# Kernel tuning notes

Measured on AMD Instinct MI355X. Metric: run time of the kernel, lower is better.

## Reference

```python
import jax, jax.numpy as jnp
import numpy as np

IN_CH, HID, OUT_CH = 1, 16, 1

def _conv(x, w, b, pad):
    # x: [B,C,H,W], w: [O,I,kh,kw], b: [O]
    y = jax.lax.conv_general_dilated(
        x, w, window_strides=(1, 1), padding=[(pad, pad), (pad, pad)],
        dimension_numbers=('NCHW', 'OIHW', 'NCHW'))
    return y + b[None, :, None, None]

def setup_inputs() -> dict:
    key = jax.random.key(0)
    ks = jax.random.split(key, 8)
    def w_init(k, shape):
        fan_in = shape[1] * shape[2] * shape[3]
        return jax.random.normal(k, shape, dtype=jnp.float32) * (1.0 / np.sqrt(fan_in))
    B, H, W = 32, 256, 256
    return {
        'x': jax.random.normal(ks[0], (B, IN_CH, H, W), dtype=jnp.float32),
        'w_perceive': w_init(ks[1], (HID * 2, IN_CH + HID, 3, 3)),
        'b_perceive': jnp.zeros((HID * 2,), jnp.float32),
        'w_up1': w_init(ks[2], (HID, HID * 2, 1, 1)),
        'b_up1': jnp.zeros((HID,), jnp.float32),
        'w_up2': w_init(ks[3], (HID, HID, 1, 1)),
        'b_up2': jnp.zeros((HID,), jnp.float32),
        'w_tau': w_init(ks[4], (HID, IN_CH + HID * 2, 3, 3)),
        'b_tau_conv': jnp.zeros((HID,), jnp.float32),
        'b_tau': jnp.ones((1, HID, 1, 1), jnp.float32) * 1.5,
        'w_read': w_init(ks[5], (OUT_CH, HID, 1, 1)),
        'b_read': jnp.zeros((OUT_CH,), jnp.float32),
        'n_steps': 10,
    }

def reference(x, w_perceive, b_perceive, w_up1, b_up1, w_up2, b_up2,
              w_tau, b_tau_conv, b_tau, w_read, b_read, n_steps):
    B, _, H, W = x.shape
    state = jnp.zeros((B, HID, H, W), dtype=x.dtype)

    def step(state, _):
        combined = jnp.concatenate([x, state], axis=1)          # [B, in+hid, H, W]
        perception = _conv(combined, w_perceive, b_perceive, 1)  # [B, 2*hid, H, W]
        h1 = jax.nn.relu(_conv(perception, w_up1, b_up1, 0))
        delta = _conv(h1, w_up2, b_up2, 0)                       # [B, hid, H, W]
        tau_input = jnp.concatenate([x, state, delta], axis=1)  # [B, in+2*hid, H, W]
        tau_logit = _conv(tau_input, w_tau, b_tau_conv, 1) + b_tau
        beta = jnp.clip(jax.nn.sigmoid(tau_logit), 0.01, 0.99)
        return beta * state + (1.0 - beta) * delta, None

    state, _ = jax.lax.scan(step, state, None, length=n_steps)
    return jax.nn.sigmoid(_conv(state, w_read, b_read, 0))
```

## Files before the change

kernel.cpp:

```cpp
#include <hip/hip_runtime.h>
#include <hip/hip_bf16.h>
#include <math.h>


#define B_   32
#define H_   256
#define W_   256
#define PIT  40
#define XPP  260

typedef unsigned short ushort_t;
typedef __attribute__((ext_vector_type(8))) short short8;
typedef __attribute__((ext_vector_type(4))) float float4v;

__device__ __forceinline__ unsigned fbits(float f) {
    union { float f; unsigned u; } v; v.f = f; return v.u;
}
__device__ __forceinline__ ushort_t f2bu(float f) {
    return (ushort_t)((fbits(f) + 0x8000u) >> 16);
}
__device__ __forceinline__ unsigned pack2(float lo, float hi) {
    union { __hip_bfloat162 h; unsigned u; } v;
    v.h = __float22bfloat162_rn(make_float2(lo, hi));
    return v.u;
}
__device__ __forceinline__ float bu2f(ushort_t u) {
    union { unsigned i; float f; } v; v.i = ((unsigned)u) << 16; return v.f;
}
__device__ __forceinline__ float lo2f(unsigned u) {
    union { unsigned i; float f; } v; v.i = u << 16; return v.f;
}
__device__ __forceinline__ float hi2f(unsigned u) {
    union { unsigned i; float f; } v; v.i = u & 0xFFFF0000u; return v.f;
}

__global__ void prep(
    const float* __restrict__ wp,
    const float* __restrict__ wu1,
    const float* __restrict__ bu1,
    const float* __restrict__ bp,
    const float* __restrict__ wu2,
    const float* __restrict__ wt,
    const float* __restrict__ btc,
    const float* __restrict__ bt,
    ushort_t* __restrict__ wh1p,
    ushort_t* __restrict__ wu2f,
    ushort_t* __restrict__ wtxf,
    ushort_t* __restrict__ wtn,
    float* __restrict__ scal)
{
    __shared__ float Weff[16 * 153];
    const int tid = threadIdx.x;

    for (int i = tid; i < 16 * 153; i += 256) {
        int j = i / 153, rem = i % 153, c = rem / 9, t = rem % 9;
        float s = 0.f;
        for (int o = 0; o < 32; ++o)
            s += wu1[j * 32 + o] * wp[o * 153 + c * 9 + t];
        Weff[i] = s;
    }
    if (tid < 16) {
        float s = bu1[tid];
        for (int o = 0; o < 32; ++o) s += wu1[tid * 32 + o] * bp[o];
        scal[tid] = s;
    }
    if (tid < 16) scal[32 + tid] = btc[tid] + bt[tid];
    if (tid < 16) scal[48 + tid] = wt[tid * 297 + 8];
    __syncthreads();

    if (tid < 16) scal[16 + tid] = Weff[tid * 153 + 8];

    for (int i = tid; i < 4 * 64 * 8; i += 256) {
        int ii = i >> 9, lane = (i >> 3) & 63, j = i & 7;
        int n = lane & 15, kk = ((lane >> 4) << 3) + j;
        int tap = 2 * ii + (kk >> 4), ch = kk & 15;
        wh1p[i] = f2bu(Weff[n * 153 + (ch + 1) * 9 + tap]);
    }
    for (int i = tid; i < 512; i += 256) {
        int lane = i >> 3, j = i & 7;
        int n = lane & 15, k = ((lane >> 4) << 3) + j;
        float v = 0.f;
        if (k < 16)       v = Weff[n * 153 + (k + 1) * 9 + 8];
        else if (k < 24)  v = Weff[n * 153 + (k - 16)];
        else if (k == 24) v = Weff[n * 153 + 8];
        wh1p[2048 + i] = f2bu(v);
    }
    for (int i = tid; i < 512; i += 256) {
        int lane = i >> 3, j = i & 7;
        int n = lane & 15, k = ((lane >> 4) << 3) + j;
        wu2f[i] = (k < 16) ? f2bu(wu2[n * 16 + k]) : (ushort_t)0;
    }
    for (int i = tid; i < 512; i += 256) {
        int lane = i >> 3, j = i & 7;
        int n = lane & 15, k = ((lane >> 4) << 3) + j;
        wtxf[i] = (k < 8) ? f2bu(wt[n * 297 + k]) : (ushort_t)0;
    }
    for (int i = tid; i < 9 * 64 * 8; i += 256) {
        int t = i / 512, lane = (i / 8) % 64, j = i % 8;
        int n = lane & 15, k = ((lane >> 4) << 3) + j;
        int c = (k < 16) ? (17 + k) : (k - 15);
        wtn[i] = f2bu(wt[n * 297 + c * 9 + t]);
    }
}

__global__ __launch_bounds__(256) void precompute_xp8(
    const float* __restrict__ x,
    ushort_t* __restrict__ xp8)
{
    int idx = blockIdx.x * 256 + threadIdx.x;
    if (idx >= B_ * XPP * XPP) return;
    int b  = idx / (XPP * XPP), rem = idx - b * (XPP * XPP);
    int by = rem / XPP, bx = rem - by * XPP;
    int gy = by - 2, gx = bx - 2;
    const float* xb = x + (size_t)b * 65536;
    short8 v;
#pragma unroll
    for (int t = 0; t < 8; ++t) {
        int yy = gy + t / 3, xx = gx + t % 3;
        bool in = ((unsigned)yy < 256u) & ((unsigned)xx < 256u);
        v[t] = in ? (short)f2bu(xb[yy * 256 + xx]) : (short)0;
    }
    *(short8*)(xp8 + (size_t)idx * 8) = v;
}

__global__ __launch_bounds__(256) void nca_step(
    const ushort_t* __restrict__ stIn,
    ushort_t* __restrict__ stOut,
    const ushort_t* __restrict__ xp8g,
    const ushort_t* __restrict__ wh1p,
    const ushort_t* __restrict__ wu2f,
    const ushort_t* __restrict__ wtxf,
    const ushort_t* __restrict__ wtn,
    const float* __restrict__ scal,
    const float* __restrict__ bu2G,
    const float* __restrict__ wrd,
    const float* __restrict__ brd,
    float* __restrict__ outg,
    int first, int last)
{
    __shared__ ushort_t comb[400 * PIT];

    const int tid  = threadIdx.x;
    const int w    = tid >> 6, lane = tid & 63;
    const int m    = lane & 15, q = lane >> 4;
    const int och  = q * 4;
    const int flat = ((int)blockIdx.z << 8) | ((int)blockIdx.y << 4) | (int)blockIdx.x;
    const int nf   = ((flat & 7) << 10) | (flat >> 3);
    const int bxi  = nf & 15, byi = (nf >> 4) & 15, bzi = nf >> 8;
    const int gx0  = bxi * 16, gy0 = byi * 16;
    const size_t pb = (size_t)bzi * 65536;
    const size_t xpb = (size_t)bzi * (XPP * XPP);
    const short8 z8 = {0, 0, 0, 0, 0, 0, 0, 0};
    const float4v z4 = {0.f, 0.f, 0.f, 0.f};

    const bool interior = (bxi >= 1) & (bxi <= 14) & (byi >= 1) & (byi <= 14);

    short8 wh1r[5], wtnr[9];
#pragma unroll
    for (int i = 0; i < 5; ++i) wh1r[i] = *(const short8*)(wh1p + (i * 64 + lane) * 8);
#pragma unroll
    for (int t = 0; t < 9; ++t) wtnr[t] = *(const short8*)(wtn + (t * 64 + lane) * 8);
    const short8 wu2r = *(const short8*)(wu2f + lane * 8);
    const short8 wtxr = *(const short8*)(wtxf + lane * 8);

    float4v beff4, bu24, wr4, tb4, wtx84;
#pragma unroll
    for (int r = 0; r < 4; ++r) {
        beff4[r] = scal[och + r];
        tb4[r]   = scal[32 + och + r];
        wtx84[r] = scal[48 + och + r];
        bu24[r]  = bu2G[och + r];
        wr4[r]   = wrd[och + r];
    }
    const float br = brd[0];

    const int sel = q >> 1;
    int offp[4];
#pragma unroll
    for (int ii = 0; ii < 4; ++ii) {
        int tA = 2 * ii, tB = 2 * ii + 1;
        int oA = ((tA / 3) * 20 + (tA % 3)) * PIT;
        int oB = ((tB / 3) * 20 + (tB % 3)) * PIT;
        offp[ii] = sel ? oB : oA;
    }
    const int chOff = 16 + (q & 1) * 8;
    const int t8off = (2 * 20 + 2) * PIT;
    const int off5  = (q == 0) ? (t8off + 16) : (q == 1) ? (t8off + 24)
                    : (q == 2) ? 32 : (t8off + 32);

    const int bpA = ((m + (q << 5)) & 63) << 2;

    if (interior & (first == 0)) {
        for (int p = tid; p < 400; p += 256) {
            int ry = p / 20, rx = p - ry * 20;
            ushort_t* row = comb + p * PIT;
            const ushort_t* sp = stIn
                + (pb + (size_t)(gy0 + ry - 2) * 256 + (gx0 + rx - 2)) * 16;
            *(short8*)(row + 16) = *(const short8*)(sp);
            *(short8*)(row + 24) = *(const short8*)(sp + 8);
            *(short8*)(row + 32) = *(const short8*)(
                xp8g + (xpb + (size_t)(gy0 + ry) * XPP + (gx0 + rx)) * 8);
        }
    } else {
        for (int p = tid; p < 400; p += 256) {
            int ry = p / 20, rx = p - ry * 20;
            int gy = gy0 + ry - 2, gx = gx0 + rx - 2;
            ushort_t* row = comb + p * PIT;
            bool in = ((unsigned)gy < 256u) & ((unsigned)gx < 256u);
            if (in && !first) {
                const ushort_t* sp = stIn + (pb + gy * 256 + gx) * 16;
                *(short8*)(row + 16) = *(const short8*)(sp);
                *(short8*)(row + 24) = *(const short8*)(sp + 8);
            } else {
                *(short8*)(row + 16) = z8; *(short8*)(row + 24) = z8;
            }
            *(short8*)(row + 32) = *(const short8*)(
                xp8g + (xpb + (size_t)(gy0 + ry) * XPP + (gx0 + rx)) * 8);
        }
    }
    __syncthreads();

    {
        int raw = w * 16 + m;
        int py = raw / 18, px = raw - (raw / 18) * 18;
        for (int i = 0; i < 6; ++i) {
            int g = w + 4 * i; if (g >= 21) break;
            bool vld = raw < 324;
            int pyc = vld ? py : 17, pxc = vld ? px : 17;
            const ushort_t* abase = comb + (pyc * 20 + pxc) * PIT;
            float4v acc = z4;
            __builtin_amdgcn_s_setprio(1);
#pragma unroll
            for (int ii = 0; ii < 4; ++ii) {
                short8 b = *(const short8*)(abase + offp[ii] + chOff);
                acc = __builtin_amdgcn_mfma_f32_16x16x32_bf16(wh1r[ii], b, acc, 0, 0, 0);
            }
            {
                short8 b = *(const short8*)(abase + off5);
                acc = __builtin_amdgcn_mfma_f32_16x16x32_bf16(wh1r[4], b, acc, 0, 0, 0);
            }
            __builtin_amdgcn_s_setprio(0);
            uint2 hv;
            hv.x = pack2(fmaxf(acc[0] + beff4[0], 0.f),
                         fmaxf(acc[1] + beff4[1], 0.f));
            hv.y = pack2(fmaxf(acc[2] + beff4[2], 0.f),
                         fmaxf(acc[3] + beff4[3], 0.f));
            union { int i4[4]; short8 s8; } bb;
            bb.i4[0] = __builtin_amdgcn_ds_bpermute(bpA,      (int)hv.x);
            bb.i4[1] = __builtin_amdgcn_ds_bpermute(bpA,      (int)hv.y);
            bb.i4[2] = __builtin_amdgcn_ds_bpermute(bpA + 64, (int)hv.x);
            bb.i4[3] = __builtin_amdgcn_ds_bpermute(bpA + 64, (int)hv.y);
            float4v d = __builtin_amdgcn_mfma_f32_16x16x32_bf16(wu2r, bb.s8, z4, 0, 0, 0);
            uint2 dv;
            dv.x = pack2(d[0] + bu24[0], d[1] + bu24[1]);
            dv.y = pack2(d[2] + bu24[2], d[3] + bu24[3]);
            if (!interior) {
                int gy = gy0 - 1 + pyc, gx = gx0 - 1 + pxc;
                bool im = ((unsigned)gy < 256u) & ((unsigned)gx < 256u);
                if (!im) { dv.x = 0u; dv.y = 0u; }
            }
            if (vld)
                *(uint2*)(comb + ((pyc + 1) * 20 + (pxc + 1)) * PIT + och) = dv;
            raw += 64; px += 10; py += 3;
            if (px >= 18) { px -= 18; py += 1; }
        }
    }
    __syncthreads();

    {
        const int w4 = w * 4;
#define LDROW(r, dx) (*(const short8*)(comb + (((r) * 20) + (m + 1 + (dx))) * PIT + q * 8))
        short8 Ta0 = LDROW(w4 + 1, 0), Ta1 = LDROW(w4 + 1, 1), Ta2 = LDROW(w4 + 1, 2);
        short8 Tb0 = LDROW(w4 + 2, 0), Tb1 = LDROW(w4 + 2, 1), Tb2 = LDROW(w4 + 2, 2);
#pragma unroll
        for (int i = 0; i < 4; ++i) {
            int g = w4 + i;
            short8 Tc0 = LDROW(g + 3, 0), Tc1 = LDROW(g + 3, 1), Tc2 = LDROW(g + 3, 2);
            short8 bx = *(const short8*)(comb + ((g + 1) * 20 + (m + 1)) * PIT + 32);
            const ushort_t* cpx = comb + ((g + 2) * 20 + (m + 2)) * PIT;
            float x8c = bu2f(comb[((g + 3) * 20 + (m + 3)) * PIT + 32]);
            uint2 su = *(const uint2*)(cpx + 16 + och);
            uint2 du = *(const uint2*)(cpx + och);
            float4v acc = z4;
            __builtin_amdgcn_s_setprio(1);
            acc = __builtin_amdgcn_mfma_f32_16x16x32_bf16(wtnr[0], Ta0, acc, 0, 0, 0);
            acc = __builtin_amdgcn_mfma_f32_16x16x32_bf16(wtnr[1], Ta1, acc, 0, 0, 0);
            acc = __builtin_amdgcn_mfma_f32_16x16x32_bf16(wtnr[2], Ta2, acc, 0, 0, 0);
            acc = __builtin_amdgcn_mfma_f32_16x16x32_bf16(wtnr[3], Tb0, acc, 0, 0, 0);
            acc = __builtin_amdgcn_mfma_f32_16x16x32_bf16(wtnr[4], Tb1, acc, 0, 0, 0);
            acc = __builtin_amdgcn_mfma_f32_16x16x32_bf16(wtnr[5], Tb2, acc, 0, 0, 0);
            acc = __builtin_amdgcn_mfma_f32_16x16x32_bf16(wtnr[6], Tc0, acc, 0, 0, 0);
            acc = __builtin_amdgcn_mfma_f32_16x16x32_bf16(wtnr[7], Tc1, acc, 0, 0, 0);
            acc = __builtin_amdgcn_mfma_f32_16x16x32_bf16(wtnr[8], Tc2, acc, 0, 0, 0);
            acc = __builtin_amdgcn_mfma_f32_16x16x32_bf16(wtxr,   bx,  acc, 0, 0, 0);
            __builtin_amdgcn_s_setprio(0);
            int gy = gy0 + g;
            const size_t pix = pb + gy * 256 + gx0 + m;
            float sold[4] = { lo2f(su.x), hi2f(su.x), lo2f(su.y), hi2f(su.y) };
            float dvv[4]  = { lo2f(du.x), hi2f(du.x), lo2f(du.y), hi2f(du.y) };
            float sn[4];
#pragma unroll
            for (int r = 0; r < 4; ++r) {
                float tl  = acc[r] + tb4[r] + x8c * wtx84[r];
                float e   = __expf(-tl);
                float bta = __builtin_amdgcn_rcpf(1.f + e);
                bta = fminf(fmaxf(bta, 0.01f), 0.99f);
                sn[r] = dvv[r] + bta * (sold[r] - dvv[r]);
            }
            if (!last) {
                uint2 o;
                o.x = pack2(sn[0], sn[1]); o.y = pack2(sn[2], sn[3]);
                *(uint2*)(stOut + pix * 16 + och) = o;
            } else {
                float v = sn[0] * wr4[0] + sn[1] * wr4[1]
                        + sn[2] * wr4[2] + sn[3] * wr4[3];
                v += __shfl_xor(v, 16);
                v += __shfl_xor(v, 32);
                if (q == 0) {
                    float eo = __expf(-(v + br));
                    outg[pix] = __builtin_amdgcn_rcpf(1.f + eo);
                }
            }
            Ta0 = Tb0; Ta1 = Tb1; Ta2 = Tb2;
            Tb0 = Tc0; Tb1 = Tc1; Tb2 = Tc2;
        }
#undef LDROW
    }
}

extern "C" void kernel_launch(void* const* d_in, const int* in_sizes, int n_in,
                              void* d_out, int out_size, void* d_ws, size_t ws_size,
                              hipStream_t stream)
{
    const float* x          = (const float*)d_in[0];
    const float* w_perceive = (const float*)d_in[1];
    const float* b_perceive = (const float*)d_in[2];
    const float* w_up1      = (const float*)d_in[3];
    const float* b_up1      = (const float*)d_in[4];
    const float* w_up2      = (const float*)d_in[5];
    const float* b_up2      = (const float*)d_in[6];
    const float* w_tau      = (const float*)d_in[7];
    const float* b_tau_conv = (const float*)d_in[8];
    const float* b_tau      = (const float*)d_in[9];
    const float* w_read     = (const float*)d_in[10];
    const float* b_read     = (const float*)d_in[11];
    float* out = (float*)d_out;

    const size_t stateElems = (size_t)B_ * H_ * W_ * 16;
    const size_t xp8Elems   = (size_t)B_ * XPP * XPP * 8;

    ushort_t* stA  = (ushort_t*)d_ws;
    ushort_t* stB  = stA + stateElems;
    ushort_t* xp8g = stB + stateElems;
    ushort_t* wh1p = xp8g + xp8Elems;
    ushort_t* wu2f = wh1p + 2560;
    ushort_t* wtxf = wu2f + 512;
    ushort_t* wtn  = wtxf + 512;
    float*    scal = (float*)(wtn + 4608);

    const size_t needBytes = (2 * stateElems + xp8Elems
                              + 2560 + 512 + 512 + 4608) * sizeof(ushort_t)
                           + 64 * sizeof(float);
    if (ws_size < needBytes) return;

    prep<<<dim3(1), dim3(256), 0, stream>>>(
        w_perceive, w_up1, b_up1, b_perceive, w_up2, w_tau,
        b_tau_conv, b_tau, wh1p, wu2f, wtxf, wtn, scal);
    precompute_xp8<<<dim3((B_ * XPP * XPP + 255) / 256), dim3(256), 0, stream>>>(
        x, xp8g);

    ushort_t* cur = stA;
    ushort_t* nxt = stB;
    for (int s = 0; s < 10; ++s) {
        nca_step<<<dim3(16, 16, 32), dim3(256), 0, stream>>>(
            cur, nxt, xp8g, wh1p, wu2f, wtxf, wtn, scal, b_up2,
            w_read, b_read, out, (s == 0) ? 1 : 0, (s == 9) ? 1 : 0);
        ushort_t* t = cur; cur = nxt; nxt = t;
    }
}
```

Before: 731.0 us.

## Fuse two NCA steps per launch using wider halo tile in shared memory

Each launch now computes two update steps: the shared tile grows from 20x20 to 24x24 with a 4-pixel halo, the first step's state is recomputed over a 20x20 region and written back to shared memory, then the second step runs as before. This halves the number of launches and the global state reads and writes between steps. In exchange it adds redundant halo computation, more shared memory per block, and a launch_bounds occupancy hint of 3.

```diff
diff --git a/kernel.cpp b/kernel.cpp
--- a/kernel.cpp
+++ b/kernel.cpp
@@ -7,7 +7,7 @@
 #define H_   256
 #define W_   256
 #define PIT  40
-#define XPP  260
+#define XPP  264
 
 typedef unsigned short ushort_t;
 typedef __attribute__((ext_vector_type(8))) short short8;
@@ -111,7 +111,7 @@
     if (idx >= B_ * XPP * XPP) return;
     int b  = idx / (XPP * XPP), rem = idx - b * (XPP * XPP);
     int by = rem / XPP, bx = rem - by * XPP;
-    int gy = by - 2, gx = bx - 2;
+    int gy = by - 4, gx = bx - 4;
     const float* xb = x + (size_t)b * 65536;
     short8 v;
 #pragma unroll
@@ -123,7 +123,7 @@
     *(short8*)(xp8 + (size_t)idx * 8) = v;
 }
 
-__global__ __launch_bounds__(256) void nca_step(
+__global__ __launch_bounds__(256, 3) void nca_step2(
     const ushort_t* __restrict__ stIn,
     ushort_t* __restrict__ stOut,
     const ushort_t* __restrict__ xp8g,
@@ -138,7 +138,7 @@
     float* __restrict__ outg,
     int first, int last)
 {
-    __shared__ ushort_t comb[400 * PIT];
+    __shared__ ushort_t comb[576 * PIT];
 
     const int tid  = threadIdx.x;
     const int w    = tid >> 6, lane = tid & 63;
@@ -179,32 +179,31 @@
 #pragma unroll
     for (int ii = 0; ii < 4; ++ii) {
         int tA = 2 * ii, tB = 2 * ii + 1;
-        int oA = ((tA / 3) * 20 + (tA % 3)) * PIT;
-        int oB = ((tB / 3) * 20 + (tB % 3)) * PIT;
+        int oA = ((tA / 3) * 24 + (tA % 3)) * PIT;
+        int oB = ((tB / 3) * 24 + (tB % 3)) * PIT;
         offp[ii] = sel ? oB : oA;
     }
     const int chOff = 16 + (q & 1) * 8;
-    const int t8off = (2 * 20 + 2) * PIT;
+    const int t8off = (2 * 24 + 2) * PIT;
     const int off5  = (q == 0) ? (t8off + 16) : (q == 1) ? (t8off + 24)
                     : (q == 2) ? 32 : (t8off + 32);
-
     const int bpA = ((m + (q << 5)) & 63) << 2;
 
     if (interior & (first == 0)) {
-        for (int p = tid; p < 400; p += 256) {
-            int ry = p / 20, rx = p - ry * 20;
+        for (int p = tid; p < 576; p += 256) {
+            int ry = p / 24, rx = p - ry * 24;
             ushort_t* row = comb + p * PIT;
             const ushort_t* sp = stIn
-                + (pb + (size_t)(gy0 + ry - 2) * 256 + (gx0 + rx - 2)) * 16;
+                + (pb + (size_t)(gy0 + ry - 4) * 256 + (gx0 + rx - 4)) * 16;
             *(short8*)(row + 16) = *(const short8*)(sp);
             *(short8*)(row + 24) = *(const short8*)(sp + 8);
             *(short8*)(row + 32) = *(const short8*)(
                 xp8g + (xpb + (size_t)(gy0 + ry) * XPP + (gx0 + rx)) * 8);
         }
     } else {
-        for (int p = tid; p < 400; p += 256) {
-            int ry = p / 20, rx = p - ry * 20;
-            int gy = gy0 + ry - 2, gx = gx0 + rx - 2;
+        for (int p = tid; p < 576; p += 256) {
+            int ry = p / 24, rx = p - ry * 24;
+            int gy = gy0 + ry - 4, gx = gx0 + rx - 4;
             ushort_t* row = comb + p * PIT;
             bool in = ((unsigned)gy < 256u) & ((unsigned)gx < 256u);
             if (in && !first) {
@@ -222,12 +221,12 @@
 
     {
         int raw = w * 16 + m;
-        int py = raw / 18, px = raw - (raw / 18) * 18;
-        for (int i = 0; i < 6; ++i) {
-            int g = w + 4 * i; if (g >= 21) break;
-            bool vld = raw < 324;
-            int pyc = vld ? py : 17, pxc = vld ? px : 17;
-            const ushort_t* abase = comb + (pyc * 20 + pxc) * PIT;
+        int py = raw / 22, px = raw - (raw / 22) * 22;
+        for (int i = 0; i < 8; ++i) {
+            int g = w + 4 * i; if (g >= 31) break;
+            bool vld = raw < 484;
+            int pyc = vld ? py : 21, pxc = vld ? px : 21;
+            const ushort_t* abase = comb + (pyc * 24 + pxc) * PIT;
             float4v acc = z4;
             __builtin_amdgcn_s_setprio(1);
 #pragma unroll
@@ -255,12 +254,115 @@
             dv.x = pack2(d[0] + bu24[0], d[1] + bu24[1]);
             dv.y = pack2(d[2] + bu24[2], d[3] + bu24[3]);
             if (!interior) {
-                int gy = gy0 - 1 + pyc, gx = gx0 - 1 + pxc;
+                int gy = gy0 + pyc - 3, gx = gx0 + pxc - 3;
                 bool im = ((unsigned)gy < 256u) & ((unsigned)gx < 256u);
                 if (!im) { dv.x = 0u; dv.y = 0u; }
             }
             if (vld)
-                *(uint2*)(comb + ((pyc + 1) * 20 + (pxc + 1)) * PIT + och) = dv;
+                *(uint2*)(comb + ((pyc + 1) * 24 + (pxc + 1)) * PIT + och) = dv;
+            raw += 64; px += 20; py += 2;
+            if (px >= 22) { px -= 22; py += 1; }
+        }
+    }
+    __syncthreads();
+
+    uint2 sreg[7];
+    {
+        int idx = w * 16 + m;
+        int r = idx / 20, c = idx - (idx / 20) * 20;
+#pragma unroll
+        for (int i = 0; i < 7; ++i) {
+            bool vld = idx < 400;
+            int rc = vld ? r : 19, cc = vld ? c : 19;
+            const ushort_t* cb = comb + ((rc + 1) * 24 + (cc + 1)) * PIT;
+            float4v acc = z4;
+            __builtin_amdgcn_s_setprio(1);
+#pragma unroll
+            for (int t = 0; t < 9; ++t) {
+                short8 b = *(const short8*)(cb + ((t / 3) * 24 + (t % 3)) * PIT + q * 8);
+                acc = __builtin_amdgcn_mfma_f32_16x16x32_bf16(wtnr[t], b, acc, 0, 0, 0);
+            }
+            {
+                short8 bx = *(const short8*)(cb + 32);
+                acc = __builtin_amdgcn_mfma_f32_16x16x32_bf16(wtxr, bx, acc, 0, 0, 0);
+            }
+            __builtin_amdgcn_s_setprio(0);
+            const ushort_t* cpx = comb + ((rc + 2) * 24 + (cc + 2)) * PIT;
+            float x8c = bu2f(comb[((rc + 3) * 24 + (cc + 3)) * PIT + 32]);
+            uint2 su = *(const uint2*)(cpx + 16 + och);
+            uint2 du = *(const uint2*)(cpx + och);
+            float sold[4] = { lo2f(su.x), hi2f(su.x), lo2f(su.y), hi2f(su.y) };
+            float dvv[4]  = { lo2f(du.x), hi2f(du.x), lo2f(du.y), hi2f(du.y) };
+            float sn[4];
+#pragma unroll
+            for (int rr = 0; rr < 4; ++rr) {
+                float tl  = acc[rr] + tb4[rr] + x8c * wtx84[rr];
+                float e   = __expf(-tl);
+                float bta = __builtin_amdgcn_rcpf(1.f + e);
+                bta = fminf(fmaxf(bta, 0.01f), 0.99f);
+                sn[rr] = dvv[rr] + bta * (sold[rr] - dvv[rr]);
+            }
+            sreg[i].x = pack2(sn[0], sn[1]);
+            sreg[i].y = pack2(sn[2], sn[3]);
+            idx += 64; c += 4; r += 3;
+            if (c >= 20) { c -= 20; r += 1; }
+        }
+    }
+    __syncthreads();
+    {
+        int idx = w * 16 + m;
+        int r = idx / 20, c = idx - (idx / 20) * 20;
+#pragma unroll
+        for (int i = 0; i < 7; ++i) {
+            if (idx < 400)
+                *(uint2*)(comb + ((r + 2) * 24 + (c + 2)) * PIT + 16 + och) = sreg[i];
+            idx += 64; c += 4; r += 3;
+            if (c >= 20) { c -= 20; r += 1; }
+        }
+    }
+    __syncthreads();
+
+    {
+        int raw = w * 16 + m;
+        int py = raw / 18, px = raw - (raw / 18) * 18;
+        for (int i = 0; i < 6; ++i) {
+            int g = w + 4 * i; if (g >= 21) break;
+            bool vld = raw < 324;
+            int pyc = vld ? py : 17, pxc = vld ? px : 17;
+            const ushort_t* abase = comb + ((pyc + 2) * 24 + (pxc + 2)) * PIT;
+            float4v acc = z4;
+            __builtin_amdgcn_s_setprio(1);
+#pragma unroll
+            for (int ii = 0; ii < 4; ++ii) {
+                short8 b = *(const short8*)(abase + offp[ii] + chOff);
+                acc = __builtin_amdgcn_mfma_f32_16x16x32_bf16(wh1r[ii], b, acc, 0, 0, 0);
+            }
+            {
+                short8 b = *(const short8*)(abase + off5);
+                acc = __builtin_amdgcn_mfma_f32_16x16x32_bf16(wh1r[4], b, acc, 0, 0, 0);
+            }
+            __builtin_amdgcn_s_setprio(0);
+            uint2 hv;
+            hv.x = pack2(fmaxf(acc[0] + beff4[0], 0.f),
+                         fmaxf(acc[1] + beff4[1], 0.f));
+            hv.y = pack2(fmaxf(acc[2] + beff4[2], 0.f),
+                         fmaxf(acc[3] + beff4[3], 0.f));
+            union { int i4[4]; short8 s8; } bb;
+            bb.i4[0] = __builtin_amdgcn_ds_bpermute(bpA,      (int)hv.x);
+            bb.i4[1] = __builtin_amdgcn_ds_bpermute(bpA,      (int)hv.y);
+            bb.i4[2] = __builtin_amdgcn_ds_bpermute(bpA + 64, (int)hv.x);
+            bb.i4[3] = __builtin_amdgcn_ds_bpermute(bpA + 64, (int)hv.y);
+            float4v d = __builtin_amdgcn_mfma_f32_16x16x32_bf16(wu2r, bb.s8, z4, 0, 0, 0);
+            uint2 dv;
+            dv.x = pack2(d[0] + bu24[0], d[1] + bu24[1]);
+            dv.y = pack2(d[2] + bu24[2], d[3] + bu24[3]);
+            if (!interior) {
+                int gy = gy0 + pyc - 1, gx = gx0 + pxc - 1;
+                bool im = ((unsigned)gy < 256u) & ((unsigned)gx < 256u);
+                if (!im) { dv.x = 0u; dv.y = 0u; }
+            }
+            if (vld)
+                *(uint2*)(comb + ((pyc + 3) * 24 + (pxc + 3)) * PIT + och) = dv;
             raw += 64; px += 10; py += 3;
             if (px >= 18) { px -= 18; py += 1; }
         }
@@ -269,16 +371,16 @@
 
     {
         const int w4 = w * 4;
-#define LDROW(r, dx) (*(const short8*)(comb + (((r) * 20) + (m + 1 + (dx))) * PIT + q * 8))
-        short8 Ta0 = LDROW(w4 + 1, 0), Ta1 = LDROW(w4 + 1, 1), Ta2 = LDROW(w4 + 1, 2);
-        short8 Tb0 = LDROW(w4 + 2, 0), Tb1 = LDROW(w4 + 2, 1), Tb2 = LDROW(w4 + 2, 2);
+#define LDROW(rr, dx) (*(const short8*)(comb + ((rr) * 24 + (m + 3 + (dx))) * PIT + q * 8))
+        short8 Ta0 = LDROW(w4 + 3, 0), Ta1 = LDROW(w4 + 3, 1), Ta2 = LDROW(w4 + 3, 2);
+        short8 Tb0 = LDROW(w4 + 4, 0), Tb1 = LDROW(w4 + 4, 1), Tb2 = LDROW(w4 + 4, 2);
 #pragma unroll
         for (int i = 0; i < 4; ++i) {
             int g = w4 + i;
-            short8 Tc0 = LDROW(g + 3, 0), Tc1 = LDROW(g + 3, 1), Tc2 = LDROW(g + 3, 2);
-            short8 bx = *(const short8*)(comb + ((g + 1) * 20 + (m + 1)) * PIT + 32);
-            const ushort_t* cpx = comb + ((g + 2) * 20 + (m + 2)) * PIT;
-            float x8c = bu2f(comb[((g + 3) * 20 + (m + 3)) * PIT + 32]);
+            short8 Tc0 = LDROW(g + 5, 0), Tc1 = LDROW(g + 5, 1), Tc2 = LDROW(g + 5, 2);
+            short8 bx = *(const short8*)(comb + ((g + 3) * 24 + (m + 3)) * PIT + 32);
+            const ushort_t* cpx = comb + ((g + 4) * 24 + (m + 4)) * PIT;
+            float x8c = bu2f(comb[((g + 5) * 24 + (m + 5)) * PIT + 32]);
             uint2 su = *(const uint2*)(cpx + 16 + och);
             uint2 du = *(const uint2*)(cpx + och);
             float4v acc = z4;
@@ -294,18 +396,17 @@
             acc = __builtin_amdgcn_mfma_f32_16x16x32_bf16(wtnr[8], Tc2, acc, 0, 0, 0);
             acc = __builtin_amdgcn_mfma_f32_16x16x32_bf16(wtxr,   bx,  acc, 0, 0, 0);
             __builtin_amdgcn_s_setprio(0);
-            int gy = gy0 + g;
-            const size_t pix = pb + gy * 256 + gx0 + m;
+            const size_t pix = pb + (size_t)(gy0 + g) * 256 + gx0 + m;
             float sold[4] = { lo2f(su.x), hi2f(su.x), lo2f(su.y), hi2f(su.y) };
             float dvv[4]  = { lo2f(du.x), hi2f(du.x), lo2f(du.y), hi2f(du.y) };
             float sn[4];
 #pragma unroll
-            for (int r = 0; r < 4; ++r) {
-                float tl  = acc[r] + tb4[r] + x8c * wtx84[r];
+            for (int rr = 0; rr < 4; ++rr) {
+                float tl  = acc[rr] + tb4[rr] + x8c * wtx84[rr];
                 float e   = __expf(-tl);
                 float bta = __builtin_amdgcn_rcpf(1.f + e);
                 bta = fminf(fmaxf(bta, 0.01f), 0.99f);
-                sn[r] = dvv[r] + bta * (sold[r] - dvv[r]);
+                sn[rr] = dvv[rr] + bta * (sold[rr] - dvv[rr]);
             }
             if (!last) {
                 uint2 o;
@@ -371,10 +472,10 @@
 
     ushort_t* cur = stA;
     ushort_t* nxt = stB;
-    for (int s = 0; s < 10; ++s) {
-        nca_step<<<dim3(16, 16, 32), dim3(256), 0, stream>>>(
+    for (int s = 0; s < 5; ++s) {
+        nca_step2<<<dim3(16, 16, 32), dim3(256), 0, stream>>>(
             cur, nxt, xp8g, wh1p, wu2f, wtxf, wtn, scal, b_up2,
-            w_read, b_read, out, (s == 0) ? 1 : 0, (s == 9) ? 1 : 0);
+            w_read, b_read, out, (s == 0) ? 1 : 0, (s == 4) ? 1 : 0);
         ushort_t* t = cur; cur = nxt; nxt = t;
     }
 }
```

Measured after the change: 900.9 us. +23.3%, slower.
